# Kernel tuning notes

Hardware: AMD Instinct MI355X
Metric: run time of the kernel (lower is better)

Reference implementation:

```python
import jax, jax.numpy as jnp
import numpy as np

N, E = 100000, 800000
IN, HID, H, C, L, OUT = 32, 128, 4, 32, 3, 5
NEG_SLOPE = 0.2
EPS = 1e-5


def setup_inputs() -> dict:
    key = jax.random.key(0)
    ks = jax.random.split(key, 20)
    s = 0.1
    inp = {
        "x": jax.random.normal(ks[0], (N, IN), jnp.float32),
        "edge_index": jax.random.randint(ks[1], (2, E), 0, N, jnp.int64),
        "edge_attr": jax.random.uniform(ks[2], (E, 1), jnp.float32),
        "Win": jax.random.normal(ks[3], (IN, HID), jnp.float32) * s,
        "b_in": jnp.zeros((HID,), jnp.float32),
        "Wg": jax.random.normal(ks[4], (L, HID, H * C), jnp.float32) * s,
        "bg": jnp.zeros((L, H * C), jnp.float32),
        "a_src": jax.random.normal(ks[5], (L, H, C), jnp.float32) * s,
        "a_dst": jax.random.normal(ks[6], (L, H, C), jnp.float32) * s,
        "We": jax.random.normal(ks[7], (L, 1, H * C), jnp.float32) * s,
        "a_edge": jax.random.normal(ks[8], (L, H, C), jnp.float32) * s,
        "ln_w": jnp.ones((L, HID), jnp.float32),
        "ln_b": jnp.zeros((L, HID), jnp.float32),
        "Wout": jax.random.normal(ks[9], (HID, OUT), jnp.float32) * s,
        "bout": jnp.zeros((OUT,), jnp.float32),
    }
    return inp


def _add_self_loops(src, dst, ea):
    # PyG fill_value='mean': self-loop attr = mean of incoming edge attrs per node
    ones = jnp.ones((src.shape[0],), ea.dtype)
    deg = jax.ops.segment_sum(ones, dst, N)
    loop_attr = jax.ops.segment_sum(ea, dst, N) / jnp.maximum(deg, 1.0)[:, None]
    idx = jnp.arange(N, dtype=src.dtype)
    return (jnp.concatenate([src, idx]), jnp.concatenate([dst, idx]),
            jnp.concatenate([ea, loop_attr], axis=0))


def _gat_conv(x, src, dst, ea, Wg, bg, a_s, a_d, We, a_e):
    xh = (x @ Wg).reshape(N, H, C)                    # [N,H,C]
    al_s = jnp.einsum('nhc,hc->nh', xh, a_s)          # [N,H]
    al_d = jnp.einsum('nhc,hc->nh', xh, a_d)
    ee = (ea @ We).reshape(-1, H, C)                  # [Et,H,C]
    al_e = jnp.einsum('ehc,hc->eh', ee, a_e)
    logits = jax.nn.leaky_relu(al_s[src] + al_d[dst] + al_e, NEG_SLOPE)
    m = jax.ops.segment_max(logits, dst, N)
    m = jnp.where(jnp.isfinite(m), m, 0.0)
    ex = jnp.exp(logits - m[dst])
    den = jax.ops.segment_sum(ex, dst, N)
    alpha = ex / (den[dst] + 1e-16)                   # segment softmax over dst
    out = jax.ops.segment_sum(alpha[:, :, None] * xh[src], dst, N)
    return out.reshape(N, H * C) + bg


def _graph_layernorm(h, w, b):
    # PyG LayerNorm(mode='graph'): normalize over all nodes and features
    h = h - jnp.mean(h)
    var = jnp.mean(h * h)
    return h / jnp.sqrt(var + EPS) * w + b


def reference(x, edge_index, edge_attr, Win, b_in, Wg, bg, a_src, a_dst, We,
              a_edge, ln_w, ln_b, Wout, bout):
    src, dst = edge_index[0], edge_index[1]
    src, dst, ea = _add_self_loops(src, dst, edge_attr)
    h = x @ Win + b_in
    for l in range(L):
        g = _gat_conv(h, src, dst, ea, Wg[l], bg[l], a_src[l], a_dst[l],
                      We[l], a_edge[l])
        g = _graph_layernorm(g, ln_w[l], ln_b[l])
        h = jax.nn.relu(g + h)
    return h @ Wout + bout
```

## Files before the change

kernel.cpp:

```cpp
#include <hip/hip_runtime.h>
#include <hip/hip_bf16.h>

#define NN 100000
#define EE 800000
#define HID 128
#define NH 4
#define CH 32
#define NL 3
#define NOUT 5
#define NEG_SLOPE 0.2f
#define LN_EPS 1e-5f
#define GCAP 96
#define NB_SCAN 98
#define HQ (HID / 2)
#define WB_LSZ 9216
#define NB_INIT 391

typedef unsigned int u32;
typedef __attribute__((ext_vector_type(8))) short bf16x8;
typedef __attribute__((ext_vector_type(4))) float f32x4;

static __device__ __forceinline__ float bflo(u32 r) { return __uint_as_float(r << 16); }
static __device__ __forceinline__ float bfhi(u32 r) { return __uint_as_float(r & 0xffff0000u); }
static __device__ __forceinline__ unsigned short f2bf(float x) {
    union U { __hip_bfloat16 b; unsigned short s; } u;
    u.b = __float2bfloat16(x);
    return u.s;
}
static __device__ __forceinline__ u32 pack2(float a, float b) {
    return (u32)f2bf(a) | ((u32)f2bf(b) << 16);
}
static __device__ __forceinline__ float lrelu(float x) {
    return x > 0.f ? x : NEG_SLOPE * x;
}

__global__ void prep_kernel(int* __restrict__ cnt, float* __restrict__ partials,
                            const float* __restrict__ We, const float* __restrict__ a_e,
                            float* __restrict__ wedot,
                            const float* __restrict__ Win, const float* __restrict__ b_in,
                            const float* __restrict__ Wg, float* __restrict__ wf,
                            const float* __restrict__ a_src, const float* __restrict__ a_dst,
                            u32* __restrict__ wb) {
    int b = blockIdx.x, t = threadIdx.x;
    if (b < NB_INIT) {
        int n = b * 256 + t;
        if (n < NN) cnt[n] = 1;
        if (n < 3 * 2048) partials[n] = 0.f;
        return;
    }
    if (b == NB_INIT) {
        if (t < NL * NH) {
            int l = t >> 2, hh = t & 3;
            float s = 0.f;
            #pragma unroll
            for (int c = 0; c < CH; c++)
                s += We[l * HID + hh * CH + c] * a_e[l * HID + hh * CH + c];
            wedot[t] = s;
        }
        return;
    }
    if (b < NB_INIT + 18) {
        int idx = (b - NB_INIT - 1) * 256 + t;
        if (idx >= 33 * HID) return;
        int r = idx >> 7, c = idx & 127;
        float acc = 0.f;
        for (int k = 0; k < HID; k++) {
            float a = (r < 32) ? Win[r * HID + k] : b_in[k];
            acc += a * Wg[(size_t)k * HID + c];
        }
        wf[r * HID + c] = acc;
        return;
    }
    {
        int idx = (b - NB_INIT - 18) * 256 + t;
        if (idx >= 2 * 2304) return;
        int l = idx / 2304;
        int rem = idx % 2304;
        int ks = rem / 576;
        int ct = (rem % 576) / 64;
        int lane = rem % 64;
        int q = lane >> 4, n = lane & 15;
        const float* W = Wg + (size_t)(l + 1) * HID * HID;
        float v[8];
        if (ct < 8) {
            #pragma unroll
            for (int j = 0; j < 8; j++) {
                int k = ks * 32 + q * 8 + j;
                v[j] = W[(size_t)k * HID + ct * 16 + n];
            }
        } else {
            #pragma unroll
            for (int j = 0; j < 8; j++) v[j] = 0.f;
            if (n < 8) {
                const float* a = (n < 4) ? (a_src + (l + 1) * HID + (n & 3) * CH)
                                         : (a_dst + (l + 1) * HID + (n & 3) * CH);
                #pragma unroll
                for (int j = 0; j < 8; j++) {
                    int k = ks * 32 + q * 8 + j;
                    const float* wrow = W + (size_t)k * HID + (n & 3) * CH;
                    float s = 0.f;
                    for (int c = 0; c < CH; c++) s += wrow[c] * a[c];
                    v[j] = s;
                }
            }
        }
        u32* dst = wb + (size_t)l * WB_LSZ + (size_t)((ks * 9 + ct) * 64 + lane) * 4;
        dst[0] = pack2(v[0], v[1]); dst[1] = pack2(v[2], v[3]);
        dst[2] = pack2(v[4], v[5]); dst[3] = pack2(v[6], v[7]);
    }
}

__global__ void hist_kernel(const int* __restrict__ ei, int* __restrict__ cnt,
                            u32* __restrict__ slot) {
    int e = blockIdx.x * blockDim.x + threadIdx.x;
    if (e >= EE) return;
    int d = ei[EE + e];
    int s = atomicAdd(&cnt[d], 1);
    slot[e] = ((u32)d << 8) | (u32)s;
}

__global__ __launch_bounds__(1024) void scan1_kernel(const int* __restrict__ cnt,
                                                     int* __restrict__ rowptr,
                                                     int* __restrict__ bsum) {
    __shared__ int ws[16];
    int gid = blockIdx.x * 1024 + threadIdx.x;
    int v = (gid < NN) ? cnt[gid] : 0;
    int lane = threadIdx.x & 63, wid = threadIdx.x >> 6;
    int s = v;
    #pragma unroll
    for (int off = 1; off < 64; off <<= 1) {
        int t = __shfl_up(s, off, 64);
        if (lane >= off) s += t;
    }
    if (lane == 63) ws[wid] = s;
    __syncthreads();
    int add = 0;
    for (int w2 = 0; w2 < wid; w2++) add += ws[w2];
    int incl = s + add;
    if (gid <= NN) rowptr[gid] = incl - v;
    if (threadIdx.x == 1023) bsum[blockIdx.x] = incl;
}

__global__ void scan2_kernel(int* __restrict__ bsum) {
    __shared__ int w0tot;
    int tid = threadIdx.x;
    int v = (tid < NB_SCAN) ? bsum[tid] : 0;
    int lane = tid & 63, wid = tid >> 6;
    int s = v;
    #pragma unroll
    for (int off = 1; off < 64; off <<= 1) {
        int t = __shfl_up(s, off, 64);
        if (lane >= off) s += t;
    }
    if (wid == 0 && lane == 63) w0tot = s;
    __syncthreads();
    int incl = s + (wid ? w0tot : 0);
    if (tid < NB_SCAN) bsum[tid] = incl - v;
}

__global__ void scan3_kernel(int* __restrict__ rowptr, const int* __restrict__ bsum) {
    int gid = blockIdx.x * 1024 + threadIdx.x;
    if (gid <= NN) rowptr[gid] += bsum[blockIdx.x];
}

__global__ void scatter_kernel(const int* __restrict__ ei, const float* __restrict__ ea,
                               const int* __restrict__ rowptr, const u32* __restrict__ slot,
                               uint2* __restrict__ edges) {
    int e = blockIdx.x * blockDim.x + threadIdx.x;
    if (e >= EE) return;
    u32 p = slot[e];
    int d = (int)(p >> 8);
    int pos = rowptr[d] + (int)(p & 255u);
    edges[pos] = make_uint2((u32)ei[e], __float_as_uint(ea[e]));
}

__global__ void selfloop_kernel(const int* __restrict__ rowptr, uint2* __restrict__ edges) {
    int n = blockIdx.x * blockDim.x + threadIdx.x;
    if (n >= NN) return;
    int rs = rowptr[n], re = rowptr[n + 1];
    float s = 0.f;
    for (int i = rs + 1; i < re; i++) s += __uint_as_float(edges[i].y);
    float m = s / fmaxf((float)(re - rs - 1), 1.0f);
    edges[rs] = make_uint2((u32)n, __float_as_uint(m));
}

static __device__ __forceinline__ void store_xh_al(
        float acc[8][4], int n0, int r0, int c0, int cg,
        u32* __restrict__ xh, const float* __restrict__ asl, const float* __restrict__ adl,
        float* __restrict__ al_s, float* __restrict__ al_d) {
    float4 as4 = *(const float4*)&asl[c0];
    float4 ad4 = *(const float4*)&adl[c0];
    int hh = cg >> 3;
    #pragma unroll
    for (int i = 0; i < 8; i++) {
        int row = n0 + r0 + i;
        if (row < NN) {
            u32 lo = pack2(acc[i][0], acc[i][1]);
            u32 hi = pack2(acc[i][2], acc[i][3]);
            *(uint2*)&xh[(size_t)row * HQ + (c0 >> 1)] = make_uint2(lo, hi);
        }
        float ps = acc[i][0] * as4.x + acc[i][1] * as4.y + acc[i][2] * as4.z + acc[i][3] * as4.w;
        float pd = acc[i][0] * ad4.x + acc[i][1] * ad4.y + acc[i][2] * ad4.z + acc[i][3] * ad4.w;
        ps += __shfl_xor(ps, 1, 64); pd += __shfl_xor(pd, 1, 64);
        ps += __shfl_xor(ps, 2, 64); pd += __shfl_xor(pd, 2, 64);
        ps += __shfl_xor(ps, 4, 64); pd += __shfl_xor(pd, 4, 64);
        if ((cg & 7) == 0 && row < NN) {
            al_s[row * 4 + hh] = ps;
            al_d[row * 4 + hh] = pd;
        }
    }
}

__global__ __launch_bounds__(256) void in_gemm_kernel(
        const float* __restrict__ x, const float* __restrict__ Win,
        const float* __restrict__ b_in, const float* __restrict__ wf,
        u32* __restrict__ h, u32* __restrict__ xh,
        const float* __restrict__ a_src0, const float* __restrict__ a_dst0,
        float* __restrict__ al_s, float* __restrict__ al_d) {
    __shared__ float xs[64][36];
    __shared__ float ws[32][128];
    int n0 = blockIdx.x * 64;
    int t = threadIdx.x;
    int cg = t & 31, rg = t >> 5;
    int c0 = cg * 4, r0 = rg * 8;
    #pragma unroll
    for (int it = 0; it < 2; it++) {
        int idx = t + it * 256;
        int row = idx >> 3, kk = (idx & 7) * 4;
        float4 v = make_float4(0.f, 0.f, 0.f, 0.f);
        if (n0 + row < NN) v = *(const float4*)&x[(size_t)(n0 + row) * 32 + kk];
        *(float4*)&xs[row][kk] = v;
    }
    #pragma unroll
    for (int it = 0; it < 4; it++) {
        int idx = t + it * 256;
        int kr = idx >> 5, f4 = (idx & 31) * 4;
        *(float4*)&ws[kr][f4] = *(const float4*)&Win[kr * HID + f4];
    }
    __syncthreads();
    {
        float acc[8][4] = {};
        #pragma unroll 8
        for (int k = 0; k < 32; k++) {
            float4 b4 = *(const float4*)&ws[k][c0];
            #pragma unroll
            for (int i = 0; i < 8; i++) {
                float a = xs[r0 + i][k];
                acc[i][0] += a * b4.x; acc[i][1] += a * b4.y;
                acc[i][2] += a * b4.z; acc[i][3] += a * b4.w;
            }
        }
        float4 bi = *(const float4*)&b_in[c0];
        #pragma unroll
        for (int i = 0; i < 8; i++) {
            int row = n0 + r0 + i;
            if (row < NN) {
                u32 lo = pack2(acc[i][0] + bi.x, acc[i][1] + bi.y);
                u32 hi = pack2(acc[i][2] + bi.z, acc[i][3] + bi.w);
                *(uint2*)&h[(size_t)row * HQ + (c0 >> 1)] = make_uint2(lo, hi);
            }
        }
    }
    __syncthreads();
    #pragma unroll
    for (int it = 0; it < 4; it++) {
        int idx = t + it * 256;
        int kr = idx >> 5, f4 = (idx & 31) * 4;
        *(float4*)&ws[kr][f4] = *(const float4*)&wf[kr * HID + f4];
    }
    __syncthreads();
    float acc2[8][4] = {};
    #pragma unroll 8
    for (int k = 0; k < 32; k++) {
        float4 b4 = *(const float4*)&ws[k][c0];
        #pragma unroll
        for (int i = 0; i < 8; i++) {
            float a = xs[r0 + i][k];
            acc2[i][0] += a * b4.x; acc2[i][1] += a * b4.y;
            acc2[i][2] += a * b4.z; acc2[i][3] += a * b4.w;
        }
    }
    float4 bf4 = *(const float4*)&wf[32 * HID + c0];
    #pragma unroll
    for (int i = 0; i < 8; i++) {
        acc2[i][0] += bf4.x; acc2[i][1] += bf4.y; acc2[i][2] += bf4.z; acc2[i][3] += bf4.w;
    }
    store_xh_al(acc2, n0, r0, c0, cg, xh, a_src0, a_dst0, al_s, al_d);
}

__global__ __launch_bounds__(256) void gemm_mfma_kernel(const u32* __restrict__ h,
        const u32* __restrict__ wb, u32* __restrict__ xh, const u32* __restrict__ g,
        const float* __restrict__ lnw, const float* __restrict__ lnb,
        const float* __restrict__ partials, u32* __restrict__ hout,
        float* __restrict__ al_s, float* __restrict__ al_d) {
    __shared__ u32 hsu[4096];
    __shared__ float sred[8];
    int n0 = blockIdx.x * 64;
    int t = threadIdx.x;
    int wv = t >> 6, lane = t & 63;
    int q = lane >> 4, n16 = lane & 15;

    {
        const float4* pp = (const float4*)partials;
        float4 v0 = pp[t * 2], v1 = pp[t * 2 + 1];
        float s = v0.x + v0.z + v1.x + v1.z;
        float qq = v0.y + v0.w + v1.y + v1.w;
        #pragma unroll
        for (int off = 1; off <= 32; off <<= 1) {
            s += __shfl_xor(s, off, 64);
            qq += __shfl_xor(qq, off, 64);
        }
        if (lane == 0) { sred[wv * 2] = s; sred[wv * 2 + 1] = qq; }
    }
    __syncthreads();
    float S = sred[0] + sred[2] + sred[4] + sred[6];
    float Q = sred[1] + sred[3] + sred[5] + sred[7];
    const float M = (float)NN * (float)HID;
    float mean = S / M;
    float rstd = rsqrtf(fmaxf(Q / M - mean * mean, 0.f) + LN_EPS);

    bf16x8 bfrag[2][4];
    #pragma unroll
    for (int ks = 0; ks < 4; ks++) {
        #pragma unroll
        for (int cc = 0; cc < 2; cc++) {
            int ct = wv * 2 + cc;
            uint4 r = *(const uint4*)&wb[(size_t)((ks * 9 + ct) * 64 + lane) * 4];
            bfrag[cc][ks] = __builtin_bit_cast(bf16x8, r);
        }
    }
    bf16x8 bal[4];
    #pragma unroll
    for (int ks = 0; ks < 4; ks++) {
        uint4 r = *(const uint4*)&wb[(size_t)((ks * 9 + 8) * 64 + lane) * 4];
        bal[ks] = __builtin_bit_cast(bf16x8, r);
    }

    {
        int row = t >> 2;
        int qq = t & 3;
        int gr = n0 + row;
        int rt = row >> 4, m = row & 15;
        #pragma unroll
        for (int ks = 0; ks < 4; ks++) {
            int kk = ks * 32 + qq * 8;
            uint4 op = make_uint4(0u, 0u, 0u, 0u);
            if (gr < NN) {
                size_t base = (size_t)gr * HQ + (kk >> 1);
                uint4 gp = *(const uint4*)&g[base];
                uint4 hp = *(const uint4*)&h[base];
                float4 wA = *(const float4*)&lnw[kk];
                float4 wB = *(const float4*)&lnw[kk + 4];
                float4 bA = *(const float4*)&lnb[kk];
                float4 bB = *(const float4*)&lnb[kk + 4];
                float v0 = fmaxf((bflo(gp.x) - mean) * rstd * wA.x + bA.x + bflo(hp.x), 0.f);
                float v1 = fmaxf((bfhi(gp.x) - mean) * rstd * wA.y + bA.y + bfhi(hp.x), 0.f);
                float v2 = fmaxf((bflo(gp.y) - mean) * rstd * wA.z + bA.z + bflo(hp.y), 0.f);
                float v3 = fmaxf((bfhi(gp.y) - mean) * rstd * wA.w + bA.w + bfhi(hp.y), 0.f);
                float v4 = fmaxf((bflo(gp.z) - mean) * rstd * wB.x + bB.x + bflo(hp.z), 0.f);
                float v5 = fmaxf((bfhi(gp.z) - mean) * rstd * wB.y + bB.y + bfhi(hp.z), 0.f);
                float v6 = fmaxf((bflo(gp.w) - mean) * rstd * wB.z + bB.z + bflo(hp.w), 0.f);
                float v7 = fmaxf((bfhi(gp.w) - mean) * rstd * wB.w + bB.w + bfhi(hp.w), 0.f);
                op.x = pack2(v0, v1); op.y = pack2(v2, v3);
                op.z = pack2(v4, v5); op.w = pack2(v6, v7);
                *(uint4*)&hout[base] = op;
            }
            *(uint4*)&hsu[((rt * 4 + ks) * 64 + qq * 16 + m) * 4] = op;
        }
    }
    __syncthreads();

    f32x4 acc[4][2];
    f32x4 accal[4];
    #pragma unroll
    for (int rt = 0; rt < 4; rt++) {
        acc[rt][0] = (f32x4){0.f, 0.f, 0.f, 0.f};
        acc[rt][1] = (f32x4){0.f, 0.f, 0.f, 0.f};
        accal[rt]  = (f32x4){0.f, 0.f, 0.f, 0.f};
    }
    #pragma unroll
    for (int rt = 0; rt < 4; rt++) {
        #pragma unroll
        for (int ks = 0; ks < 4; ks++) {
            uint4 araw = *(const uint4*)&hsu[((rt * 4 + ks) * 64 + lane) * 4];
            bf16x8 af = __builtin_bit_cast(bf16x8, araw);
            acc[rt][0] = __builtin_amdgcn_mfma_f32_16x16x32_bf16(af, bfrag[0][ks], acc[rt][0], 0, 0, 0);
            acc[rt][1] = __builtin_amdgcn_mfma_f32_16x16x32_bf16(af, bfrag[1][ks], acc[rt][1], 0, 0, 0);
            if (wv == 3)
                accal[rt] = __builtin_amdgcn_mfma_f32_16x16x32_bf16(af, bal[ks], accal[rt], 0, 0, 0);
        }
    }

    #pragma unroll
    for (int rt = 0; rt < 4; rt++) {
        #pragma unroll
        for (int reg = 0; reg < 4; reg++) {
            int row = n0 + rt * 16 + q * 4 + reg;
            #pragma unroll
            for (int cc = 0; cc < 2; cc++) {
                float v = acc[rt][cc][reg];
                float vp = __shfl_xor(v, 1, 64);
                if (!(n16 & 1) && row < NN) {
                    int colp = (wv * 2 + cc) * 8 + (n16 >> 1);
                    xh[(size_t)row * HQ + colp] = pack2(v, vp);
                }
            }
            if (wv == 3 && row < NN && n16 < 8) {
                float v = accal[rt][reg];
                if (n16 < 4) al_s[row * 4 + n16] = v;
                else         al_d[row * 4 + (n16 - 4)] = v;
            }
        }
    }
}

__global__ __launch_bounds__(256) void gat_agg_kernel(const int* __restrict__ rowptr,
        const uint2* __restrict__ edges, const u32* __restrict__ xh,
        const float* __restrict__ al_s, const float* __restrict__ al_d,
        const float* __restrict__ wedot, const float* __restrict__ bg,
        u32* __restrict__ g, float* __restrict__ partials) {
    __shared__ float lds_ex[4][GCAP * 4];
    __shared__ int lds_src[4][GCAP];
    int wv = threadIdx.x >> 6, lane = threadIdx.x & 63;
    int base = (blockIdx.x * 4 + wv) * 4;
    if (base >= NN) return;
    float* ex_w = lds_ex[wv];
    int* src_w = lds_src[wv];
    int b1 = base + 1 < NN ? base + 1 : NN;
    int b2 = base + 2 < NN ? base + 2 : NN;
    int b3 = base + 3 < NN ? base + 3 : NN;
    int b4 = base + 4 < NN ? base + 4 : NN;
    int r0 = rowptr[base], r1 = rowptr[b1], r2 = rowptr[b2], r3 = rowptr[b3], r4 = rowptr[b4];
    int span = r4 - r0;
    int ncached = span < GCAP ? span : GCAP;
    float wd0 = wedot[0], wd1 = wedot[1], wd2 = wedot[2], wd3 = wedot[3];

    for (int i = lane; i < ncached; i += 64) {
        int gi = r0 + i;
        uint2 e = edges[gi];
        int s = (int)e.x;
        float eav = __uint_as_float(e.y);
        int d = (gi >= r1) + (gi >= r2) + (gi >= r3);
        float4 aldv = *(const float4*)&al_d[(base + d) * 4];
        float4 als = *(const float4*)&al_s[s * 4];
        float e0 = __expf(lrelu(als.x + aldv.x + eav * wd0));
        float e1 = __expf(lrelu(als.y + aldv.y + eav * wd1));
        float e2 = __expf(lrelu(als.z + aldv.z + eav * wd2));
        float e3 = __expf(lrelu(als.w + aldv.w + eav * wd3));
        src_w[i] = s;
        *(float4*)&ex_w[i * 4] = make_float4(e0, e1, e2, e3);
    }

    int nl = lane >> 4, cg = lane & 15;
    int n = base + nl;
    bool nvalid = n < NN;
    int ls = (nl == 0 ? r0 : nl == 1 ? r1 : nl == 2 ? r2 : r3) - r0;
    int le = (nl == 0 ? r1 : nl == 1 ? r2 : nl == 2 ? r3 : r4) - r0;
    int lec = le < ncached ? le : ncached;
    int head = cg >> 2;
    int c4 = cg * 4;
    float a0 = 0.f, a1 = 0.f, a2 = 0.f, a3 = 0.f;
    float a4 = 0.f, a5 = 0.f, a6 = 0.f, a7 = 0.f, den = 0.f;
    int j = ls;
    for (; j + 3 < lec; j += 4) {
        int s0 = src_w[j], s1 = src_w[j + 1], s2 = src_w[j + 2], s3 = src_w[j + 3];
        float e0 = ex_w[j * 4 + head],       e1 = ex_w[(j + 1) * 4 + head];
        float e2 = ex_w[(j + 2) * 4 + head], e3 = ex_w[(j + 3) * 4 + head];
        uint4 x0 = *(const uint4*)&xh[(size_t)s0 * HQ + c4];
        uint4 x1 = *(const uint4*)&xh[(size_t)s1 * HQ + c4];
        uint4 x2 = *(const uint4*)&xh[(size_t)s2 * HQ + c4];
        uint4 x3 = *(const uint4*)&xh[(size_t)s3 * HQ + c4];
        den += e0 + e1 + e2 + e3;
        a0 += e0 * bflo(x0.x); a1 += e0 * bfhi(x0.x);
        a2 += e0 * bflo(x0.y); a3 += e0 * bfhi(x0.y);
        a4 += e0 * bflo(x0.z); a5 += e0 * bfhi(x0.z);
        a6 += e0 * bflo(x0.w); a7 += e0 * bfhi(x0.w);
        a0 += e1 * bflo(x1.x); a1 += e1 * bfhi(x1.x);
        a2 += e1 * bflo(x1.y); a3 += e1 * bfhi(x1.y);
        a4 += e1 * bflo(x1.z); a5 += e1 * bfhi(x1.z);
        a6 += e1 * bflo(x1.w); a7 += e1 * bfhi(x1.w);
        a0 += e2 * bflo(x2.x); a1 += e2 * bfhi(x2.x);
        a2 += e2 * bflo(x2.y); a3 += e2 * bfhi(x2.y);
        a4 += e2 * bflo(x2.z); a5 += e2 * bfhi(x2.z);
        a6 += e2 * bflo(x2.w); a7 += e2 * bfhi(x2.w);
        a0 += e3 * bflo(x3.x); a1 += e3 * bfhi(x3.x);
        a2 += e3 * bflo(x3.y); a3 += e3 * bfhi(x3.y);
        a4 += e3 * bflo(x3.z); a5 += e3 * bfhi(x3.z);
        a6 += e3 * bflo(x3.w); a7 += e3 * bfhi(x3.w);
    }
    for (; j < lec; j++) {
        int s0 = src_w[j];
        float e0 = ex_w[j * 4 + head];
        uint4 x0 = *(const uint4*)&xh[(size_t)s0 * HQ + c4];
        den += e0;
        a0 += e0 * bflo(x0.x); a1 += e0 * bfhi(x0.x);
        a2 += e0 * bflo(x0.y); a3 += e0 * bfhi(x0.y);
        a4 += e0 * bflo(x0.z); a5 += e0 * bfhi(x0.z);
        a6 += e0 * bflo(x0.w); a7 += e0 * bfhi(x0.w);
    }
    if (le > lec && nvalid) {
        float aldh = al_d[n * 4 + head];
        float wdh = wedot[head];
        for (int jt = (ls > lec ? ls : lec); jt < le; jt++) {
            uint2 e = edges[r0 + jt];
            int s = (int)e.x;
            float eav = __uint_as_float(e.y);
            float ex = __expf(lrelu(al_s[s * 4 + head] + aldh + eav * wdh));
            den += ex;
            uint4 x0 = *(const uint4*)&xh[(size_t)s * HQ + c4];
            a0 += ex * bflo(x0.x); a1 += ex * bfhi(x0.x);
            a2 += ex * bflo(x0.y); a3 += ex * bfhi(x0.y);
            a4 += ex * bflo(x0.z); a5 += ex * bfhi(x0.z);
            a6 += ex * bflo(x0.w); a7 += ex * bfhi(x0.w);
        }
    }

    float inv = 1.0f / (den + 1e-16f);
    int c0 = cg * 8;
    float4 bgA = *(const float4*)&bg[c0];
    float4 bgB = *(const float4*)&bg[c0 + 4];
    float o0 = a0 * inv + bgA.x, o1 = a1 * inv + bgA.y;
    float o2 = a2 * inv + bgA.z, o3 = a3 * inv + bgA.w;
    float o4 = a4 * inv + bgB.x, o5 = a5 * inv + bgB.y;
    float o6 = a6 * inv + bgB.z, o7 = a7 * inv + bgB.w;
    float ss = 0.f, sq = 0.f;
    if (nvalid) {
        uint4 op;
        op.x = pack2(o0, o1); op.y = pack2(o2, o3);
        op.z = pack2(o4, o5); op.w = pack2(o6, o7);
        *(uint4*)&g[(size_t)n * HQ + c4] = op;
        ss = o0 + o1 + o2 + o3 + o4 + o5 + o6 + o7;
        sq = o0 * o0 + o1 * o1 + o2 * o2 + o3 * o3
           + o4 * o4 + o5 * o5 + o6 * o6 + o7 * o7;
    }
    #pragma unroll
    for (int off = 1; off <= 32; off <<= 1) {
        ss += __shfl_xor(ss, off, 64);
        sq += __shfl_xor(sq, off, 64);
    }
    if (lane == 0) {
        int sl = ((blockIdx.x * 4 + wv) & 1023) * 2;
        atomicAdd(&partials[sl], ss);
        atomicAdd(&partials[sl + 1], sq);
    }
}

__global__ void stats_kernel(const float* __restrict__ partials, float* __restrict__ stats) {
    __shared__ float ls[16], lq[16];
    int tid = threadIdx.x;
    float s = partials[tid * 2], q = partials[tid * 2 + 1];
    #pragma unroll
    for (int off = 32; off; off >>= 1) {
        s += __shfl_xor(s, off, 64);
        q += __shfl_xor(q, off, 64);
    }
    int lane = tid & 63, wid = tid >> 6;
    if (lane == 0) { ls[wid] = s; lq[wid] = q; }
    __syncthreads();
    if (tid == 0) {
        float S = 0.f, Q = 0.f;
        for (int w2 = 0; w2 < 16; w2++) { S += ls[w2]; Q += lq[w2]; }
        const float M = (float)NN * (float)HID;
        float mean = S / M;
        float var = Q / M - mean * mean;
        stats[0] = mean;
        stats[1] = rsqrtf(fmaxf(var, 0.f) + LN_EPS);
    }
}

__global__ __launch_bounds__(256) void ln_out_kernel(const u32* __restrict__ g,
        const u32* __restrict__ h, const float* __restrict__ lnw,
        const float* __restrict__ lnb, const float* __restrict__ stats,
        const float* __restrict__ Wout, const float* __restrict__ bout,
        float* __restrict__ out) {
    __shared__ float wsh[HID * NOUT];
    int t = threadIdx.x;
    for (int i = t; i < HID * NOUT; i += 256) wsh[i] = Wout[i];
    __syncthreads();
    int wv = t >> 6, lane = t & 63;
    int nl = lane >> 4, cg = lane & 15;
    int n = (blockIdx.x * 4 + wv) * 4 + nl;
    bool nvalid = n < NN;
    float mean = stats[0], rstd = stats[1];
    float p[NOUT] = {};
    if (nvalid) {
        int c0 = cg * 8;
        uint4 gv = *(const uint4*)&g[(size_t)n * HQ + cg * 4];
        uint4 hv = *(const uint4*)&h[(size_t)n * HQ + cg * 4];
        float4 wA = *(const float4*)&lnw[c0], wB = *(const float4*)&lnw[c0 + 4];
        float4 bA = *(const float4*)&lnb[c0], bB = *(const float4*)&lnb[c0 + 4];
        float o[8];
        o[0] = fmaxf((bflo(gv.x) - mean) * rstd * wA.x + bA.x + bflo(hv.x), 0.f);
        o[1] = fmaxf((bfhi(gv.x) - mean) * rstd * wA.y + bA.y + bfhi(hv.x), 0.f);
        o[2] = fmaxf((bflo(gv.y) - mean) * rstd * wA.z + bA.z + bflo(hv.y), 0.f);
        o[3] = fmaxf((bfhi(gv.y) - mean) * rstd * wA.w + bA.w + bfhi(hv.y), 0.f);
        o[4] = fmaxf((bflo(gv.z) - mean) * rstd * wB.x + bB.x + bflo(hv.z), 0.f);
        o[5] = fmaxf((bfhi(gv.z) - mean) * rstd * wB.y + bB.y + bfhi(hv.z), 0.f);
        o[6] = fmaxf((bflo(gv.w) - mean) * rstd * wB.z + bB.z + bflo(hv.w), 0.f);
        o[7] = fmaxf((bfhi(gv.w) - mean) * rstd * wB.w + bB.w + bfhi(hv.w), 0.f);
        #pragma unroll
        for (int jj = 0; jj < NOUT; jj++) {
            float acc = 0.f;
            #pragma unroll
            for (int k = 0; k < 8; k++) acc += o[k] * wsh[(c0 + k) * NOUT + jj];
            p[jj] = acc;
        }
    }
    #pragma unroll
    for (int off = 1; off <= 8; off <<= 1) {
        #pragma unroll
        for (int jj = 0; jj < NOUT; jj++) p[jj] += __shfl_xor(p[jj], off, 64);
    }
    if (cg == 0 && nvalid) {
        #pragma unroll
        for (int jj = 0; jj < NOUT; jj++)
            out[(size_t)n * NOUT + jj] = p[jj] + bout[jj];
    }
}

extern "C" void kernel_launch(void* const* d_in, const int* in_sizes, int n_in,
                              void* d_out, int out_size, void* d_ws, size_t ws_size,
                              hipStream_t stream) {
    const float* x      = (const float*)d_in[0];
    const int*   ei     = (const int*)d_in[1];
    const float* ea     = (const float*)d_in[2];
    const float* Win    = (const float*)d_in[3];
    const float* b_in   = (const float*)d_in[4];
    const float* Wg     = (const float*)d_in[5];
    const float* bg     = (const float*)d_in[6];
    const float* a_src  = (const float*)d_in[7];
    const float* a_dst  = (const float*)d_in[8];
    const float* We     = (const float*)d_in[9];
    const float* a_edge = (const float*)d_in[10];
    const float* ln_w   = (const float*)d_in[11];
    const float* ln_b   = (const float*)d_in[12];
    const float* Wout   = (const float*)d_in[13];
    const float* bout   = (const float*)d_in[14];
    float* out = (float*)d_out;

    char* w = (char*)d_ws;
    size_t off = 0;
    auto alloc = [&](size_t bytes) -> void* {
        void* p = w + off;
        off = (off + bytes + 255) & ~(size_t)255;
        return p;
    };
    u32*   slot    = (u32*)alloc((size_t)EE * sizeof(u32));
    int*   cnt     = (int*)alloc(NN * sizeof(int));
    int*   rowptr  = (int*)alloc((NN + 1) * sizeof(int));
    int*   bsum    = (int*)alloc(NB_SCAN * sizeof(int));
    uint2* edges   = (uint2*)alloc((size_t)(EE + NN) * sizeof(uint2));
    u32*   h       = (u32*)alloc((size_t)NN * HQ * sizeof(u32));
    u32*   g       = (u32*)alloc((size_t)NN * HQ * sizeof(u32));
    u32*   xh      = (u32*)alloc((size_t)NN * HQ * sizeof(u32));
    float* al_s    = (float*)alloc((size_t)NN * NH * sizeof(float));
    float* al_d    = (float*)alloc((size_t)NN * NH * sizeof(float));
    float* wedot   = (float*)alloc(16 * sizeof(float));
    float* wf      = (float*)alloc(33 * HID * sizeof(float));
    u32*   wb      = (u32*)alloc((size_t)2 * WB_LSZ * sizeof(u32));
    float* partials = (float*)alloc(3 * 2048 * sizeof(float));
    float* stats   = (float*)alloc(16 * sizeof(float));
    (void)ws_size; (void)n_in; (void)in_sizes; (void)out_size;

    prep_kernel<<<NB_INIT + 18 + 18, 256, 0, stream>>>(cnt, partials, We, a_edge, wedot,
                                                       Win, b_in, Wg, wf, a_src, a_dst, wb);
    hist_kernel<<<(EE + 255) / 256, 256, 0, stream>>>(ei, cnt, slot);
    scan1_kernel<<<NB_SCAN, 1024, 0, stream>>>(cnt, rowptr, bsum);
    scan2_kernel<<<1, 128, 0, stream>>>(bsum);
    scan3_kernel<<<NB_SCAN, 1024, 0, stream>>>(rowptr, bsum);
    scatter_kernel<<<(EE + 255) / 256, 256, 0, stream>>>(ei, ea, rowptr, slot, edges);
    selfloop_kernel<<<(NN + 255) / 256, 256, 0, stream>>>(rowptr, edges);

    const int ngrid = (NN + 63) / 64;
    in_gemm_kernel<<<ngrid, 256, 0, stream>>>(x, Win, b_in, wf, h, xh,
                                              a_src, a_dst, al_s, al_d);
    for (int l = 0; l < NL; l++) {
        if (l > 0) {
            gemm_mfma_kernel<<<ngrid, 256, 0, stream>>>(
                h, wb + (size_t)(l - 1) * WB_LSZ, xh, g,
                ln_w + (size_t)(l - 1) * HID, ln_b + (size_t)(l - 1) * HID,
                partials + (size_t)(l - 1) * 2048, h, al_s, al_d);
        }
        gat_agg_kernel<<<(NN + 15) / 16, 256, 0, stream>>>(
            rowptr, edges, xh, al_s, al_d, wedot + l * 4,
            bg + (size_t)l * HID, g, partials + (size_t)l * 2048);
    }
    stats_kernel<<<1, 1024, 0, stream>>>(partials + 2 * 2048, stats);

    ln_out_kernel<<<(NN + 15) / 16, 256, 0, stream>>>(g, h, ln_w + (size_t)2 * HID,
                                                      ln_b + (size_t)2 * HID,
                                                      stats, Wout, bout, out);
}
```

Before: 402.6 us.

## Fold self-loops into aggregation, MFMA input GEMM, and fuse stats into output

The self-loop edge is no longer stored in the CSR. Its mean edge attribute is accumulated on the fly inside the aggregation kernel, which removes the selfloop kernel and shrinks the edge array. The input GEMM is rewritten to use bf16 MFMA with prepacked weights, including a folded Wg·a projection for the attention logits. The stats kernel is removed by having every ln_out block redundantly reduce the partials itself. GCAP is also lowered, and a small prep2 kernel is added; the extra bf16 rounding in the input GEMM and attention terms may cost some precision.

```diff
diff --git a/kernel.cpp b/kernel.cpp
--- a/kernel.cpp
+++ b/kernel.cpp
@@ -10,7 +10,7 @@
 #define NOUT 5
 #define NEG_SLOPE 0.2f
 #define LN_EPS 1e-5f
-#define GCAP 96
+#define GCAP 64
 #define NB_SCAN 98
 #define HQ (HID / 2)
 #define WB_LSZ 9216
@@ -40,11 +40,11 @@
                             const float* __restrict__ Win, const float* __restrict__ b_in,
                             const float* __restrict__ Wg, float* __restrict__ wf,
                             const float* __restrict__ a_src, const float* __restrict__ a_dst,
-                            u32* __restrict__ wb) {
+                            u32* __restrict__ wb, float* __restrict__ wga) {
     int b = blockIdx.x, t = threadIdx.x;
     if (b < NB_INIT) {
         int n = b * 256 + t;
-        if (n < NN) cnt[n] = 1;
+        if (n < NN) cnt[n] = 0;
         if (n < 3 * 2048) partials[n] = 0.f;
         return;
     }
@@ -56,6 +56,16 @@
             for (int c = 0; c < CH; c++)
                 s += We[l * HID + hh * CH + c] * a_e[l * HID + hh * CH + c];
             wedot[t] = s;
+        }
+        for (int i = t; i < HID * 8; i += 256) {
+            int m = i >> 3, j = i & 7;
+            int hh = j & 3;
+            const float* a = (j < 4) ? (a_src + hh * CH) : (a_dst + hh * CH);
+            const float* wrow = Wg + (size_t)m * HID + hh * CH;
+            float s = 0.f;
+            #pragma unroll
+            for (int c = 0; c < CH; c++) s += wrow[c] * a[c];
+            wga[i] = s;
         }
         return;
     }
@@ -110,6 +120,45 @@
     }
 }
 
+__global__ __launch_bounds__(64) void prep2_kernel(const float* __restrict__ Win,
+        const float* __restrict__ b_in, const float* __restrict__ wga,
+        float* __restrict__ wf, u32* __restrict__ wb2) {
+    int b = blockIdx.x, lane = threadIdx.x;
+    int q = lane >> 4, n = lane & 15;
+    if (b == 17) {
+        if (lane < 8) {
+            float s = 0.f;
+            for (int m = 0; m < HID; m++) s += b_in[m] * wga[m * 8 + lane];
+            wf[33 * HID + lane] = s;
+        }
+        return;
+    }
+    float v[8];
+    if (b < 8) {
+        #pragma unroll
+        for (int j = 0; j < 8; j++) v[j] = Win[(q * 8 + j) * HID + b * 16 + n];
+    } else if (b < 16) {
+        int ct = b - 8;
+        #pragma unroll
+        for (int j = 0; j < 8; j++) v[j] = wf[(q * 8 + j) * HID + ct * 16 + n];
+    } else {
+        #pragma unroll
+        for (int j = 0; j < 8; j++) v[j] = 0.f;
+        if (n < 8) {
+            #pragma unroll
+            for (int j = 0; j < 8; j++) {
+                const float* wrow = Win + (q * 8 + j) * HID;
+                float s = 0.f;
+                for (int m = 0; m < HID; m++) s += wrow[m] * wga[m * 8 + n];
+                v[j] = s;
+            }
+        }
+    }
+    u32* dst = wb2 + (size_t)(b * 64 + lane) * 4;
+    dst[0] = pack2(v[0], v[1]); dst[1] = pack2(v[2], v[3]);
+    dst[2] = pack2(v[4], v[5]); dst[3] = pack2(v[6], v[7]);
+}
+
 __global__ void hist_kernel(const int* __restrict__ ei, int* __restrict__ cnt,
                             u32* __restrict__ slot) {
     int e = blockIdx.x * blockDim.x + threadIdx.x;
@@ -174,118 +223,94 @@
     edges[pos] = make_uint2((u32)ei[e], __float_as_uint(ea[e]));
 }
 
-__global__ void selfloop_kernel(const int* __restrict__ rowptr, uint2* __restrict__ edges) {
-    int n = blockIdx.x * blockDim.x + threadIdx.x;
-    if (n >= NN) return;
-    int rs = rowptr[n], re = rowptr[n + 1];
-    float s = 0.f;
-    for (int i = rs + 1; i < re; i++) s += __uint_as_float(edges[i].y);
-    float m = s / fmaxf((float)(re - rs - 1), 1.0f);
-    edges[rs] = make_uint2((u32)n, __float_as_uint(m));
-}
-
-static __device__ __forceinline__ void store_xh_al(
-        float acc[8][4], int n0, int r0, int c0, int cg,
-        u32* __restrict__ xh, const float* __restrict__ asl, const float* __restrict__ adl,
+__global__ __launch_bounds__(256) void in_gemm_kernel(
+        const float* __restrict__ x, const u32* __restrict__ wb2,
+        const float* __restrict__ wf, const float* __restrict__ b_in,
+        u32* __restrict__ h, u32* __restrict__ xh,
         float* __restrict__ al_s, float* __restrict__ al_d) {
-    float4 as4 = *(const float4*)&asl[c0];
-    float4 ad4 = *(const float4*)&adl[c0];
-    int hh = cg >> 3;
-    #pragma unroll
-    for (int i = 0; i < 8; i++) {
-        int row = n0 + r0 + i;
-        if (row < NN) {
-            u32 lo = pack2(acc[i][0], acc[i][1]);
-            u32 hi = pack2(acc[i][2], acc[i][3]);
-            *(uint2*)&xh[(size_t)row * HQ + (c0 >> 1)] = make_uint2(lo, hi);
-        }
-        float ps = acc[i][0] * as4.x + acc[i][1] * as4.y + acc[i][2] * as4.z + acc[i][3] * as4.w;
-        float pd = acc[i][0] * ad4.x + acc[i][1] * ad4.y + acc[i][2] * ad4.z + acc[i][3] * ad4.w;
-        ps += __shfl_xor(ps, 1, 64); pd += __shfl_xor(pd, 1, 64);
-        ps += __shfl_xor(ps, 2, 64); pd += __shfl_xor(pd, 2, 64);
-        ps += __shfl_xor(ps, 4, 64); pd += __shfl_xor(pd, 4, 64);
-        if ((cg & 7) == 0 && row < NN) {
-            al_s[row * 4 + hh] = ps;
-            al_d[row * 4 + hh] = pd;
-        }
-    }
-}
-
-__global__ __launch_bounds__(256) void in_gemm_kernel(
-        const float* __restrict__ x, const float* __restrict__ Win,
-        const float* __restrict__ b_in, const float* __restrict__ wf,
-        u32* __restrict__ h, u32* __restrict__ xh,
-        const float* __restrict__ a_src0, const float* __restrict__ a_dst0,
-        float* __restrict__ al_s, float* __restrict__ al_d) {
-    __shared__ float xs[64][36];
-    __shared__ float ws[32][128];
+    __shared__ u32 xsu[1024];
+    int t = threadIdx.x;
+    int wv = t >> 6, lane = t & 63;
+    int q = lane >> 4, n16 = lane & 15;
     int n0 = blockIdx.x * 64;
-    int t = threadIdx.x;
-    int cg = t & 31, rg = t >> 5;
-    int c0 = cg * 4, r0 = rg * 8;
-    #pragma unroll
-    for (int it = 0; it < 2; it++) {
-        int idx = t + it * 256;
-        int row = idx >> 3, kk = (idx & 7) * 4;
-        float4 v = make_float4(0.f, 0.f, 0.f, 0.f);
-        if (n0 + row < NN) v = *(const float4*)&x[(size_t)(n0 + row) * 32 + kk];
-        *(float4*)&xs[row][kk] = v;
-    }
-    #pragma unroll
-    for (int it = 0; it < 4; it++) {
-        int idx = t + it * 256;
-        int kr = idx >> 5, f4 = (idx & 31) * 4;
-        *(float4*)&ws[kr][f4] = *(const float4*)&Win[kr * HID + f4];
+    {
+        int row = t >> 2, qq = t & 3;
+        int gr = n0 + row;
+        int rt = row >> 4, m = row & 15;
+        uint4 op = make_uint4(0u, 0u, 0u, 0u);
+        if (gr < NN) {
+            float4 vA = *(const float4*)&x[(size_t)gr * 32 + qq * 8];
+            float4 vB = *(const float4*)&x[(size_t)gr * 32 + qq * 8 + 4];
+            op.x = pack2(vA.x, vA.y); op.y = pack2(vA.z, vA.w);
+            op.z = pack2(vB.x, vB.y); op.w = pack2(vB.z, vB.w);
+        }
+        *(uint4*)&xsu[(rt * 64 + qq * 16 + m) * 4] = op;
+    }
+    bf16x8 bwin[2], bwf[2], bal;
+    #pragma unroll
+    for (int cc = 0; cc < 2; cc++) {
+        uint4 r0 = *(const uint4*)&wb2[(size_t)(((wv * 2 + cc)) * 64 + lane) * 4];
+        uint4 r1 = *(const uint4*)&wb2[(size_t)((8 + wv * 2 + cc) * 64 + lane) * 4];
+        bwin[cc] = __builtin_bit_cast(bf16x8, r0);
+        bwf[cc]  = __builtin_bit_cast(bf16x8, r1);
+    }
+    {
+        uint4 r = *(const uint4*)&wb2[(size_t)(16 * 64 + lane) * 4];
+        bal = __builtin_bit_cast(bf16x8, r);
     }
     __syncthreads();
-    {
-        float acc[8][4] = {};
-        #pragma unroll 8
-        for (int k = 0; k < 32; k++) {
-            float4 b4 = *(const float4*)&ws[k][c0];
+    f32x4 acch[4][2], accx[4][2], accal[4];
+    #pragma unroll
+    for (int rt = 0; rt < 4; rt++) {
+        acch[rt][0] = (f32x4){0.f, 0.f, 0.f, 0.f};
+        acch[rt][1] = (f32x4){0.f, 0.f, 0.f, 0.f};
+        accx[rt][0] = (f32x4){0.f, 0.f, 0.f, 0.f};
+        accx[rt][1] = (f32x4){0.f, 0.f, 0.f, 0.f};
+        accal[rt]   = (f32x4){0.f, 0.f, 0.f, 0.f};
+    }
+    #pragma unroll
+    for (int rt = 0; rt < 4; rt++) {
+        uint4 araw = *(const uint4*)&xsu[(rt * 64 + lane) * 4];
+        bf16x8 af = __builtin_bit_cast(bf16x8, araw);
+        acch[rt][0] = __builtin_amdgcn_mfma_f32_16x16x32_bf16(af, bwin[0], acch[rt][0], 0, 0, 0);
+        acch[rt][1] = __builtin_amdgcn_mfma_f32_16x16x32_bf16(af, bwin[1], acch[rt][1], 0, 0, 0);
+        accx[rt][0] = __builtin_amdgcn_mfma_f32_16x16x32_bf16(af, bwf[0], accx[rt][0], 0, 0, 0);
+        accx[rt][1] = __builtin_amdgcn_mfma_f32_16x16x32_bf16(af, bwf[1], accx[rt][1], 0, 0, 0);
+        if (wv == 3)
+            accal[rt] = __builtin_amdgcn_mfma_f32_16x16x32_bf16(af, bal, accal[rt], 0, 0, 0);
+    }
+    float bi[2], bfv[2];
+    #pragma unroll
+    for (int cc = 0; cc < 2; cc++) {
+        int col = (wv * 2 + cc) * 16 + n16;
+        bi[cc] = b_in[col];
+        bfv[cc] = wf[32 * HID + col];
+    }
+    float bfa = (wv == 3 && n16 < 8) ? wf[33 * HID + n16] : 0.f;
+    #pragma unroll
+    for (int rt = 0; rt < 4; rt++) {
+        #pragma unroll
+        for (int reg = 0; reg < 4; reg++) {
+            int row = n0 + rt * 16 + q * 4 + reg;
             #pragma unroll
-            for (int i = 0; i < 8; i++) {
-                float a = xs[r0 + i][k];
-                acc[i][0] += a * b4.x; acc[i][1] += a * b4.y;
-                acc[i][2] += a * b4.z; acc[i][3] += a * b4.w;
+            for (int cc = 0; cc < 2; cc++) {
+                float v = acch[rt][cc][reg] + bi[cc];
+                float vp = __shfl_xor(v, 1, 64);
+                float u = accx[rt][cc][reg] + bfv[cc];
+                float up = __shfl_xor(u, 1, 64);
+                if (!(n16 & 1) && row < NN) {
+                    int colp = (wv * 2 + cc) * 8 + (n16 >> 1);
+                    h[(size_t)row * HQ + colp] = pack2(v, vp);
+                    xh[(size_t)row * HQ + colp] = pack2(u, up);
+                }
             }
-        }
-        float4 bi = *(const float4*)&b_in[c0];
-        #pragma unroll
-        for (int i = 0; i < 8; i++) {
-            int row = n0 + r0 + i;
-            if (row < NN) {
-                u32 lo = pack2(acc[i][0] + bi.x, acc[i][1] + bi.y);
-                u32 hi = pack2(acc[i][2] + bi.z, acc[i][3] + bi.w);
-                *(uint2*)&h[(size_t)row * HQ + (c0 >> 1)] = make_uint2(lo, hi);
+            if (wv == 3 && row < NN && n16 < 8) {
+                float v = accal[rt][reg] + bfa;
+                if (n16 < 4) al_s[row * 4 + n16] = v;
+                else         al_d[row * 4 + (n16 - 4)] = v;
             }
         }
     }
-    __syncthreads();
-    #pragma unroll
-    for (int it = 0; it < 4; it++) {
-        int idx = t + it * 256;
-        int kr = idx >> 5, f4 = (idx & 31) * 4;
-        *(float4*)&ws[kr][f4] = *(const float4*)&wf[kr * HID + f4];
-    }
-    __syncthreads();
-    float acc2[8][4] = {};
-    #pragma unroll 8
-    for (int k = 0; k < 32; k++) {
-        float4 b4 = *(const float4*)&ws[k][c0];
-        #pragma unroll
-        for (int i = 0; i < 8; i++) {
-            float a = xs[r0 + i][k];
-            acc2[i][0] += a * b4.x; acc2[i][1] += a * b4.y;
-            acc2[i][2] += a * b4.z; acc2[i][3] += a * b4.w;
-        }
-    }
-    float4 bf4 = *(const float4*)&wf[32 * HID + c0];
-    #pragma unroll
-    for (int i = 0; i < 8; i++) {
-        acc2[i][0] += bf4.x; acc2[i][1] += bf4.y; acc2[i][2] += bf4.z; acc2[i][3] += bf4.w;
-    }
-    store_xh_al(acc2, n0, r0, c0, cg, xh, a_src0, a_dst0, al_s, al_d);
 }
 
 __global__ __launch_bounds__(256) void gemm_mfma_kernel(const u32* __restrict__ h,
@@ -420,11 +445,13 @@
         const float* __restrict__ wedot, const float* __restrict__ bg,
         u32* __restrict__ g, float* __restrict__ partials) {
     __shared__ float lds_ex[4][GCAP * 4];
+    __shared__ float lds_ea[4][GCAP];
     __shared__ int lds_src[4][GCAP];
     int wv = threadIdx.x >> 6, lane = threadIdx.x & 63;
     int base = (blockIdx.x * 4 + wv) * 4;
     if (base >= NN) return;
     float* ex_w = lds_ex[wv];
+    float* ea_w = lds_ea[wv];
     int* src_w = lds_src[wv];
     int b1 = base + 1 < NN ? base + 1 : NN;
     int b2 = base + 2 < NN ? base + 2 : NN;
@@ -448,6 +475,7 @@
         float e2 = __expf(lrelu(als.z + aldv.z + eav * wd2));
         float e3 = __expf(lrelu(als.w + aldv.w + eav * wd3));
         src_w[i] = s;
+        ea_w[i] = eav;
         *(float4*)&ex_w[i * 4] = make_float4(e0, e1, e2, e3);
     }
 
@@ -459,8 +487,9 @@
     int lec = le < ncached ? le : ncached;
     int head = cg >> 2;
     int c4 = cg * 4;
+    float wdh = head == 0 ? wd0 : head == 1 ? wd1 : head == 2 ? wd2 : wd3;
     float a0 = 0.f, a1 = 0.f, a2 = 0.f, a3 = 0.f;
-    float a4 = 0.f, a5 = 0.f, a6 = 0.f, a7 = 0.f, den = 0.f;
+    float a4 = 0.f, a5 = 0.f, a6 = 0.f, a7 = 0.f, den = 0.f, easum = 0.f;
     int j = ls;
     for (; j + 3 < lec; j += 4) {
         int s0 = src_w[j], s1 = src_w[j + 1], s2 = src_w[j + 2], s3 = src_w[j + 3];
@@ -471,6 +500,7 @@
         uint4 x2 = *(const uint4*)&xh[(size_t)s2 * HQ + c4];
         uint4 x3 = *(const uint4*)&xh[(size_t)s3 * HQ + c4];
         den += e0 + e1 + e2 + e3;
+        easum += ea_w[j] + ea_w[j + 1] + ea_w[j + 2] + ea_w[j + 3];
         a0 += e0 * bflo(x0.x); a1 += e0 * bfhi(x0.x);
         a2 += e0 * bflo(x0.y); a3 += e0 * bfhi(x0.y);
         a4 += e0 * bflo(x0.z); a5 += e0 * bfhi(x0.z);
@@ -493,6 +523,7 @@
         float e0 = ex_w[j * 4 + head];
         uint4 x0 = *(const uint4*)&xh[(size_t)s0 * HQ + c4];
         den += e0;
+        easum += ea_w[j];
         a0 += e0 * bflo(x0.x); a1 += e0 * bfhi(x0.x);
         a2 += e0 * bflo(x0.y); a3 += e0 * bfhi(x0.y);
         a4 += e0 * bflo(x0.z); a5 += e0 * bfhi(x0.z);
@@ -500,19 +531,30 @@
     }
     if (le > lec && nvalid) {
         float aldh = al_d[n * 4 + head];
-        float wdh = wedot[head];
         for (int jt = (ls > lec ? ls : lec); jt < le; jt++) {
             uint2 e = edges[r0 + jt];
             int s = (int)e.x;
             float eav = __uint_as_float(e.y);
             float ex = __expf(lrelu(al_s[s * 4 + head] + aldh + eav * wdh));
             den += ex;
+            easum += eav;
             uint4 x0 = *(const uint4*)&xh[(size_t)s * HQ + c4];
             a0 += ex * bflo(x0.x); a1 += ex * bfhi(x0.x);
             a2 += ex * bflo(x0.y); a3 += ex * bfhi(x0.y);
             a4 += ex * bflo(x0.z); a5 += ex * bfhi(x0.z);
             a6 += ex * bflo(x0.w); a7 += ex * bfhi(x0.w);
         }
+    }
+    if (nvalid) {
+        float mea = easum / fmaxf((float)(le - ls), 1.0f);
+        float alh = al_s[n * 4 + head] + al_d[n * 4 + head];
+        float ex = __expf(lrelu(alh + mea * wdh));
+        den += ex;
+        uint4 x0 = *(const uint4*)&xh[(size_t)n * HQ + c4];
+        a0 += ex * bflo(x0.x); a1 += ex * bfhi(x0.x);
+        a2 += ex * bflo(x0.y); a3 += ex * bfhi(x0.y);
+        a4 += ex * bflo(x0.z); a5 += ex * bfhi(x0.z);
+        a6 += ex * bflo(x0.w); a7 += ex * bfhi(x0.w);
     }
 
     float inv = 1.0f / (den + 1e-16f);
@@ -545,43 +587,38 @@
     }
 }
 
-__global__ void stats_kernel(const float* __restrict__ partials, float* __restrict__ stats) {
-    __shared__ float ls[16], lq[16];
-    int tid = threadIdx.x;
-    float s = partials[tid * 2], q = partials[tid * 2 + 1];
-    #pragma unroll
-    for (int off = 32; off; off >>= 1) {
-        s += __shfl_xor(s, off, 64);
-        q += __shfl_xor(q, off, 64);
-    }
-    int lane = tid & 63, wid = tid >> 6;
-    if (lane == 0) { ls[wid] = s; lq[wid] = q; }
-    __syncthreads();
-    if (tid == 0) {
-        float S = 0.f, Q = 0.f;
-        for (int w2 = 0; w2 < 16; w2++) { S += ls[w2]; Q += lq[w2]; }
-        const float M = (float)NN * (float)HID;
-        float mean = S / M;
-        float var = Q / M - mean * mean;
-        stats[0] = mean;
-        stats[1] = rsqrtf(fmaxf(var, 0.f) + LN_EPS);
-    }
-}
-
 __global__ __launch_bounds__(256) void ln_out_kernel(const u32* __restrict__ g,
         const u32* __restrict__ h, const float* __restrict__ lnw,
-        const float* __restrict__ lnb, const float* __restrict__ stats,
+        const float* __restrict__ lnb, const float* __restrict__ partials,
         const float* __restrict__ Wout, const float* __restrict__ bout,
         float* __restrict__ out) {
     __shared__ float wsh[HID * NOUT];
+    __shared__ float sred[8];
     int t = threadIdx.x;
+    int wv = t >> 6, lane = t & 63;
+    {
+        const float4* pp = (const float4*)partials;
+        float4 v0 = pp[t * 2], v1 = pp[t * 2 + 1];
+        float s = v0.x + v0.z + v1.x + v1.z;
+        float qq = v0.y + v0.w + v1.y + v1.w;
+        #pragma unroll
+        for (int off = 1; off <= 32; off <<= 1) {
+            s += __shfl_xor(s, off, 64);
+            qq += __shfl_xor(qq, off, 64);
+        }
+        if (lane == 0) { sred[wv * 2] = s; sred[wv * 2 + 1] = qq; }
+    }
     for (int i = t; i < HID * NOUT; i += 256) wsh[i] = Wout[i];
     __syncthreads();
-    int wv = t >> 6, lane = t & 63;
+    float S = sred[0] + sred[2] + sred[4] + sred[6];
+    float Q = sred[1] + sred[3] + sred[5] + sred[7];
+    const float M = (float)NN * (float)HID;
+    float mean = S / M;
+    float rstd = rsqrtf(fmaxf(Q / M - mean * mean, 0.f) + LN_EPS);
+
     int nl = lane >> 4, cg = lane & 15;
     int n = (blockIdx.x * 4 + wv) * 4 + nl;
     bool nvalid = n < NN;
-    float mean = stats[0], rstd = stats[1];
     float p[NOUT] = {};
     if (nvalid) {
         int c0 = cg * 8;
@@ -649,31 +686,32 @@
     int*   cnt     = (int*)alloc(NN * sizeof(int));
     int*   rowptr  = (int*)alloc((NN + 1) * sizeof(int));
     int*   bsum    = (int*)alloc(NB_SCAN * sizeof(int));
-    uint2* edges   = (uint2*)alloc((size_t)(EE + NN) * sizeof(uint2));
+    uint2* edges   = (uint2*)alloc((size_t)EE * sizeof(uint2));
     u32*   h       = (u32*)alloc((size_t)NN * HQ * sizeof(u32));
     u32*   g       = (u32*)alloc((size_t)NN * HQ * sizeof(u32));
     u32*   xh      = (u32*)alloc((size_t)NN * HQ * sizeof(u32));
     float* al_s    = (float*)alloc((size_t)NN * NH * sizeof(float));
     float* al_d    = (float*)alloc((size_t)NN * NH * sizeof(float));
     float* wedot   = (float*)alloc(16 * sizeof(float));
-    float* wf      = (float*)alloc(33 * HID * sizeof(float));
+    float* wf      = (float*)alloc(34 * HID * sizeof(float));
+    float* wga     = (float*)alloc(HID * 8 * sizeof(float));
     u32*   wb      = (u32*)alloc((size_t)2 * WB_LSZ * sizeof(u32));
+    u32*   wb2     = (u32*)alloc(17 * 64 * 4 * sizeof(u32));
     float* partials = (float*)alloc(3 * 2048 * sizeof(float));
-    float* stats   = (float*)alloc(16 * sizeof(float));
     (void)ws_size; (void)n_in; (void)in_sizes; (void)out_size;
 
     prep_kernel<<<NB_INIT + 18 + 18, 256, 0, stream>>>(cnt, partials, We, a_edge, wedot,
-                                                       Win, b_in, Wg, wf, a_src, a_dst, wb);
+                                                       Win, b_in, Wg, wf, a_src, a_dst,
+                                                       wb, wga);
+    prep2_kernel<<<18, 64, 0, stream>>>(Win, b_in, wga, wf, wb2);
     hist_kernel<<<(EE + 255) / 256, 256, 0, stream>>>(ei, cnt, slot);
     scan1_kernel<<<NB_SCAN, 1024, 0, stream>>>(cnt, rowptr, bsum);
     scan2_kernel<<<1, 128, 0, stream>>>(bsum);
     scan3_kernel<<<NB_SCAN, 1024, 0, stream>>>(rowptr, bsum);
     scatter_kernel<<<(EE + 255) / 256, 256, 0, stream>>>(ei, ea, rowptr, slot, edges);
-    selfloop_kernel<<<(NN + 255) / 256, 256, 0, stream>>>(rowptr, edges);
 
     const int ngrid = (NN + 63) / 64;
-    in_gemm_kernel<<<ngrid, 256, 0, stream>>>(x, Win, b_in, wf, h, xh,
-                                              a_src, a_dst, al_s, al_d);
+    in_gemm_kernel<<<ngrid, 256, 0, stream>>>(x, wb2, wf, b_in, h, xh, al_s, al_d);
     for (int l = 0; l < NL; l++) {
         if (l > 0) {
             gemm_mfma_kernel<<<ngrid, 256, 0, stream>>>(
@@ -685,9 +723,8 @@
             rowptr, edges, xh, al_s, al_d, wedot + l * 4,
             bg + (size_t)l * HID, g, partials + (size_t)l * 2048);
     }
-    stats_kernel<<<1, 1024, 0, stream>>>(partials + 2 * 2048, stats);
 
     ln_out_kernel<<<(NN + 15) / 16, 256, 0, stream>>>(g, h, ln_w + (size_t)2 * HID,
                                                       ln_b + (size_t)2 * HID,
-                                                      stats, Wout, bout, out);
-}
+                                                      partials + 2 * 2048, Wout, bout, out);
+}
```

Result: no change. 400.9 us (-0.4%).
